# Optimization experiments

Hardware: AMD Instinct MI355X
Metric: run time of the kernel (lower is better)

The kernel has to match this reference:

```python
import jax, jax.numpy as jnp
import numpy as np

B, T, IN, H, NC = 256, 512, 64, 512, 64
H2 = H // 2


def setup_inputs() -> dict:
    key = jax.random.key(0)
    ks = jax.random.split(key, 13)
    s = 0.05
    return {
        "x": jax.random.normal(ks[0], (B, T, IN), jnp.float32),
        # layer 0 LSTM weights (PyTorch layout: [4H, in], gate order i,f,g,o)
        "w_ih0": jax.random.normal(ks[1], (4 * H, IN), jnp.float32) * s,
        "w_hh0": jax.random.normal(ks[2], (4 * H, H), jnp.float32) * s,
        "b_ih0": jax.random.normal(ks[3], (4 * H,), jnp.float32) * s,
        "b_hh0": jax.random.normal(ks[4], (4 * H,), jnp.float32) * s,
        # layer 1 LSTM weights
        "w_ih1": jax.random.normal(ks[5], (4 * H, H), jnp.float32) * s,
        "w_hh1": jax.random.normal(ks[6], (4 * H, H), jnp.float32) * s,
        "b_ih1": jax.random.normal(ks[7], (4 * H,), jnp.float32) * s,
        "b_hh1": jax.random.normal(ks[8], (4 * H,), jnp.float32) * s,
        # classifier head
        "w1": jax.random.normal(ks[9], (H2, H), jnp.float32) * s,
        "b1": jax.random.normal(ks[10], (H2,), jnp.float32) * s,
        "w2": jax.random.normal(ks[11], (NC, H2), jnp.float32) * s,
        "b2": jax.random.normal(ks[12], (NC,), jnp.float32) * s,
    }


def _lstm_layer(x, w_ih, w_hh, b_ih, b_hh):
    # x: [B, T, D_in] -> hidden sequence [B, T, H]
    b, t, _ = x.shape
    h_dim = w_hh.shape[1]
    # precompute input projection for all time steps: [B, T, 4H]
    gx = jnp.einsum('btd,gd->btg', x, w_ih) + b_ih + b_hh

    def step(carry, g_t):
        h, c = carry
        gates = g_t + h @ w_hh.T  # [B, 4H]
        i, f, g, o = jnp.split(gates, 4, axis=-1)
        i = jax.nn.sigmoid(i)
        f = jax.nn.sigmoid(f)
        g = jnp.tanh(g)
        o = jax.nn.sigmoid(o)
        c_new = f * c + i * g
        h_new = o * jnp.tanh(c_new)
        return (h_new, c_new), h_new

    h0 = jnp.zeros((b, h_dim), x.dtype)
    c0 = jnp.zeros((b, h_dim), x.dtype)
    (_, _), hs = jax.lax.scan(step, (h0, c0), jnp.swapaxes(gx, 0, 1))
    return jnp.swapaxes(hs, 0, 1)  # [B, T, H]


def reference(x, w_ih0, w_hh0, b_ih0, b_hh0, w_ih1, w_hh1, b_ih1, b_hh1, w1, b1, w2, b2):
    # 2-layer LSTM (eval mode: inter-layer dropout disabled)
    out = _lstm_layer(x, w_ih0, w_hh0, b_ih0, b_hh0)
    out = _lstm_layer(out, w_ih1, w_hh1, b_ih1, b_hh1)
    feat = out[:, -1, :]  # last time step hidden state [B, H]
    # classifier: Linear -> ReLU -> (Dropout off in eval) -> Linear
    hmid = jax.nn.relu(feat @ w1.T + b1)
    logits = hmid @ w2.T + b2
    return logits
```

## Files before the change

### kernel.cpp

```cpp
#include <hip/hip_runtime.h>
#include <stdint.h>

#define B_  256
#define T_  512
#define IN_ 64
#define H_  512
#define G4_ 2048
#define NC_ 64
#define H2_ 256

typedef _Float16 f16;
typedef __attribute__((ext_vector_type(4))) _Float16 f16x4;
typedef __attribute__((ext_vector_type(4))) float    f32x4;
typedef __attribute__((ext_vector_type(4))) unsigned int u32x4;

__device__ __forceinline__ float sigf(float x) {
  return __builtin_amdgcn_rcpf(1.0f + __expf(-x));
}
__device__ __forceinline__ float tanh_fast(float x) {
  x = fminf(fmaxf(x, -15.f), 15.f);
  const float e = __expf(2.f * x);
  return (e - 1.f) * __builtin_amdgcn_rcpf(e + 1.f);
}

__device__ __forceinline__ void store_u32_l3(void* p, unsigned v) {
  asm volatile("global_store_dword %0, %1, off sc0 sc1" :: "v"(p), "v"(v) : "memory");
}
__device__ __forceinline__ unsigned load_u32_l3(const void* p) {
  unsigned r;
  asm volatile("global_load_dword %0, %1, off sc0 sc1" : "=v"(r) : "v"(p) : "memory");
  return r;
}
__device__ __forceinline__ u32x4 load_u32x4_l3(const void* p) {
  u32x4 r;
  asm volatile("global_load_dwordx4 %0, %1, off sc0 sc1" : "=v"(r) : "v"(p) : "memory");
  return r;
}
__device__ __forceinline__ void wait_vm0() {
  asm volatile("s_waitcnt vmcnt(0)" ::: "memory");
}

__global__ void cvt_f32_f16(const float* __restrict__ s, f16* __restrict__ d, int n) {
  int i = blockIdx.x * blockDim.x + threadIdx.x;
  int st = gridDim.x * blockDim.x;
  for (; i < n; i += st) d[i] = (f16)s[i];
}

__global__ void bias_comb(const float* __restrict__ a, const float* __restrict__ b,
                          float* __restrict__ d, int n) {
  int i = blockIdx.x * blockDim.x + threadIdx.x;
  if (i < n) d[i] = a[i] + b[i];
}

__global__ __launch_bounds__(512, 2) void fused_g(
    const f16* __restrict__ x16,
    const f16* __restrict__ wih0,
    const f16* __restrict__ whh0,
    const f16* __restrict__ wih1,
    const f16* __restrict__ whh1,
    const float* __restrict__ bias0,
    const float* __restrict__ bias1,
    f16* __restrict__ h0seq,
    f16* __restrict__ hbuf1,
    unsigned* __restrict__ flags) {
  __shared__ __align__(16) unsigned char smem[50688];
  const int bid = blockIdx.x;
  const int tid = threadIdx.x;
  const int lane = tid & 63, wv = tid >> 6;
  const int l15 = lane & 15, hi = lane >> 4;

  if (bid < 128) {
    const int grp = bid >> 3, sl = bid & 7;
    f16 (*xt)[72]   = (f16(*)[72])smem;
    f16 (*ht)[532]  = (f16(*)[532])(smem + 2304);
    float (*gl)[260] = (float(*)[260])(smem + 2304 + 17024);

    int gidx[2]; f16x4 bhh[2][32]; f16x4 bih[2][4]; float bv[2];
#pragma unroll
    for (int nt = 0; nt < 2; ++nt) {
      const int lg = (wv * 2 + nt) * 16 + l15;
      const int grow = (lg >> 6) * H_ + sl * 64 + (lg & 63);
      gidx[nt] = grow; bv[nt] = bias0[grow];
      const f16* wp = whh0 + (size_t)grow * H_;
#pragma unroll
      for (int ks = 0; ks < 32; ++ks) bhh[nt][ks] = *(const f16x4*)(wp + ks * 16 + 4 * hi);
      const f16* wq = wih0 + (size_t)grow * IN_;
#pragma unroll
      for (int ks = 0; ks < 4; ++ks) bih[nt][ks] = *(const f16x4*)(wq + ks * 16 + 4 * hi);
    }

    const int bl = tid >> 5;
    const int j0 = (tid & 31) * 2;
    float c0 = 0.f, c1 = 0.f;
    const int hrow = tid >> 5, hcol = (tid & 31) * 16;

    for (int t = 0; t < T_; ++t) {
      if (tid < 128) {
        const f16* xs = x16 + ((size_t)(grp * 16 + (tid >> 3)) * T_ + t) * IN_ + (tid & 7) * 8;
        *(uint4*)&xt[tid >> 3][(tid & 7) * 8] = *(const uint4*)xs;
      }
      if (t != 0) {
        const unsigned* pp = flags + (size_t)(grp * 8 + (lane & 7)) * 16;
        const unsigned want = (unsigned)t;
        for (;;) {
          unsigned v = load_u32_l3(pp); wait_vm0();
          if (__all((int)(v >= want))) break;
          __builtin_amdgcn_s_sleep(1);
        }
        const f16* hs = h0seq + ((size_t)(t - 1) * B_ + grp * 16 + hrow) * H_ + hcol;
        u32x4 r0 = load_u32x4_l3(hs);
        u32x4 r1 = load_u32x4_l3(hs + 8);
        wait_vm0();
        __builtin_amdgcn_sched_barrier(0);
        *(u32x4*)&ht[hrow][hcol]     = r0;
        *(u32x4*)&ht[hrow][hcol + 8] = r1;
      } else {
        u32x4 z = {0u, 0u, 0u, 0u};
        *(u32x4*)&ht[hrow][hcol]     = z;
        *(u32x4*)&ht[hrow][hcol + 8] = z;
      }
      __syncthreads();

      f32x4 acc[2];
#pragma unroll
      for (int nt = 0; nt < 2; ++nt) { acc[nt][0] = bv[nt]; acc[nt][1] = bv[nt]; acc[nt][2] = bv[nt]; acc[nt][3] = bv[nt]; }
#pragma unroll
      for (int ks = 0; ks < 4; ++ks) {
        const f16x4 a = *(const f16x4*)&xt[l15][ks * 16 + 4 * hi];
        acc[0] = __builtin_amdgcn_mfma_f32_16x16x16f16(a, bih[0][ks], acc[0], 0, 0, 0);
        acc[1] = __builtin_amdgcn_mfma_f32_16x16x16f16(a, bih[1][ks], acc[1], 0, 0, 0);
      }
#pragma unroll
      for (int ks = 0; ks < 32; ++ks) {
        const f16x4 a = *(const f16x4*)&ht[l15][ks * 16 + 4 * hi];
        acc[0] = __builtin_amdgcn_mfma_f32_16x16x16f16(a, bhh[0][ks], acc[0], 0, 0, 0);
        acc[1] = __builtin_amdgcn_mfma_f32_16x16x16f16(a, bhh[1][ks], acc[1], 0, 0, 0);
      }
#pragma unroll
      for (int nt = 0; nt < 2; ++nt) {
        const int col = (wv * 2 + nt) * 16 + l15;
#pragma unroll
        for (int r = 0; r < 4; ++r) gl[4 * hi + r][col] = acc[nt][r];
      }
      __syncthreads();

      const float gi = gl[bl][j0],        gi1 = gl[bl][j0 + 1];
      const float gf = gl[bl][64 + j0],   gf1 = gl[bl][64 + j0 + 1];
      const float gg = gl[bl][128 + j0],  gg1 = gl[bl][128 + j0 + 1];
      const float go = gl[bl][192 + j0],  go1 = gl[bl][192 + j0 + 1];
      c0 = sigf(gf) * c0 + sigf(gi) * tanh_fast(gg);
      c1 = sigf(gf1) * c1 + sigf(gi1) * tanh_fast(gg1);
      const f16 h0h = (f16)(sigf(go) * tanh_fast(c0));
      const f16 h1h = (f16)(sigf(go1) * tanh_fast(c1));
      unsigned hp = ((unsigned)__builtin_bit_cast(unsigned short, h1h) << 16)
                  |  (unsigned)__builtin_bit_cast(unsigned short, h0h);
      store_u32_l3(h0seq + ((size_t)t * B_ + grp * 16 + bl) * H_ + sl * 64 + j0, hp);
      wait_vm0();
      __syncthreads();
      if (tid == 0) store_u32_l3(flags + (size_t)(grp * 8 + sl) * 16, (unsigned)(t + 1));
    }

  } else {
    const int grp = (bid - 128) >> 3, sl = (bid - 128) & 7;
    f16 (*ht0)[532]  = (f16(*)[532])smem;
    f16 (*ht1)[532]  = (f16(*)[532])(smem + 17024);
    float (*gl)[260] = (float(*)[260])(smem + 34048);

    int gidx[2]; f16x4 bih[2][32]; f16x4 bhh[2][32]; float bv[2];
#pragma unroll
    for (int nt = 0; nt < 2; ++nt) {
      const int lg = (wv * 2 + nt) * 16 + l15;
      const int grow = (lg >> 6) * H_ + sl * 64 + (lg & 63);
      gidx[nt] = grow; bv[nt] = bias1[grow];
      const f16* wp = wih1 + (size_t)grow * H_;
#pragma unroll
      for (int ks = 0; ks < 32; ++ks) bih[nt][ks] = *(const f16x4*)(wp + ks * 16 + 4 * hi);
      const f16* wq = whh1 + (size_t)grow * H_;
#pragma unroll
      for (int ks = 0; ks < 32; ++ks) bhh[nt][ks] = *(const f16x4*)(wq + ks * 16 + 4 * hi);
    }

    const int bl = tid >> 5;
    const int j0 = (tid & 31) * 2;
    float c0 = 0.f, c1 = 0.f;
    const int hrow = tid >> 5, hcol = (tid & 31) * 16;

    for (int t = 0; t < T_; ++t) {
      {
        const bool isOwn = (lane >= 8 && lane < 16);
        const int slot = isOwn ? (128 + grp * 8 + (lane - 8)) : (grp * 8 + (lane & 7));
        const unsigned want = isOwn ? (unsigned)t : (unsigned)(t + 1);
        const unsigned* pp = flags + (size_t)slot * 16;
        for (;;) {
          unsigned v = load_u32_l3(pp); wait_vm0();
          if (__all((int)(v >= want))) break;
          __builtin_amdgcn_s_sleep(1);
        }
      }
      {
        const f16* hs0 = h0seq + ((size_t)t * B_ + grp * 16 + hrow) * H_ + hcol;
        u32x4 r0 = load_u32x4_l3(hs0);
        u32x4 r1 = load_u32x4_l3(hs0 + 8);
        if (t != 0) {
          const f16* hs1 = hbuf1 + ((size_t)((t - 1) & 1) * B_ + grp * 16 + hrow) * H_ + hcol;
          u32x4 r2 = load_u32x4_l3(hs1);
          u32x4 r3 = load_u32x4_l3(hs1 + 8);
          wait_vm0();
          __builtin_amdgcn_sched_barrier(0);
          *(u32x4*)&ht1[hrow][hcol]     = r2;
          *(u32x4*)&ht1[hrow][hcol + 8] = r3;
        } else {
          wait_vm0();
          __builtin_amdgcn_sched_barrier(0);
          u32x4 z = {0u, 0u, 0u, 0u};
          *(u32x4*)&ht1[hrow][hcol]     = z;
          *(u32x4*)&ht1[hrow][hcol + 8] = z;
        }
        *(u32x4*)&ht0[hrow][hcol]     = r0;
        *(u32x4*)&ht0[hrow][hcol + 8] = r1;
      }
      __syncthreads();

      f32x4 acc[2];
#pragma unroll
      for (int nt = 0; nt < 2; ++nt) { acc[nt][0] = bv[nt]; acc[nt][1] = bv[nt]; acc[nt][2] = bv[nt]; acc[nt][3] = bv[nt]; }
#pragma unroll
      for (int ks = 0; ks < 32; ++ks) {
        const f16x4 a0 = *(const f16x4*)&ht0[l15][ks * 16 + 4 * hi];
        acc[0] = __builtin_amdgcn_mfma_f32_16x16x16f16(a0, bih[0][ks], acc[0], 0, 0, 0);
        acc[1] = __builtin_amdgcn_mfma_f32_16x16x16f16(a0, bih[1][ks], acc[1], 0, 0, 0);
      }
#pragma unroll
      for (int ks = 0; ks < 32; ++ks) {
        const f16x4 a1 = *(const f16x4*)&ht1[l15][ks * 16 + 4 * hi];
        acc[0] = __builtin_amdgcn_mfma_f32_16x16x16f16(a1, bhh[0][ks], acc[0], 0, 0, 0);
        acc[1] = __builtin_amdgcn_mfma_f32_16x16x16f16(a1, bhh[1][ks], acc[1], 0, 0, 0);
      }
#pragma unroll
      for (int nt = 0; nt < 2; ++nt) {
        const int col = (wv * 2 + nt) * 16 + l15;
#pragma unroll
        for (int r = 0; r < 4; ++r) gl[4 * hi + r][col] = acc[nt][r];
      }
      __syncthreads();

      const float gi = gl[bl][j0],        gi1 = gl[bl][j0 + 1];
      const float gf = gl[bl][64 + j0],   gf1 = gl[bl][64 + j0 + 1];
      const float gg = gl[bl][128 + j0],  gg1 = gl[bl][128 + j0 + 1];
      const float go = gl[bl][192 + j0],  go1 = gl[bl][192 + j0 + 1];
      c0 = sigf(gf) * c0 + sigf(gi) * tanh_fast(gg);
      c1 = sigf(gf1) * c1 + sigf(gi1) * tanh_fast(gg1);
      const f16 ha = (f16)(sigf(go) * tanh_fast(c0));
      const f16 hb = (f16)(sigf(go1) * tanh_fast(c1));
      unsigned hp = ((unsigned)__builtin_bit_cast(unsigned short, hb) << 16)
                  |  (unsigned)__builtin_bit_cast(unsigned short, ha);
      store_u32_l3(hbuf1 + ((size_t)(t & 1) * B_ + grp * 16 + bl) * H_ + sl * 64 + j0, hp);
      wait_vm0();
      __syncthreads();
      if (tid == 0) store_u32_l3(flags + (size_t)(128 + grp * 8 + sl) * 16, (unsigned)(t + 1));
    }
  }
}

__global__ void head_g(const f16* __restrict__ h1, const float* __restrict__ w1,
                       const float* __restrict__ b1, const float* __restrict__ w2,
                       const float* __restrict__ b2, float* __restrict__ out) {
  __shared__ float ft[512];
  __shared__ float hm[256];
  const int b = blockIdx.x, tid = threadIdx.x;
  ft[tid * 2]     = (float)h1[(size_t)b * H_ + tid * 2];
  ft[tid * 2 + 1] = (float)h1[(size_t)b * H_ + tid * 2 + 1];
  __syncthreads();
  {
    float d = b1[tid];
    const float* wr = w1 + (size_t)tid * H_;
#pragma unroll 8
    for (int k = 0; k < H_; ++k) d += ft[k] * wr[k];
    hm[tid] = fmaxf(d, 0.f);
  }
  __syncthreads();
  if (tid < NC_) {
    float d = b2[tid];
    const float* wr = w2 + (size_t)tid * H2_;
#pragma unroll 8
    for (int k = 0; k < H2_; ++k) d += hm[k] * wr[k];
    out[(size_t)b * NC_ + tid] = d;
  }
}

extern "C" void kernel_launch(void* const* d_in, const int* in_sizes, int n_in,
                              void* d_out, int out_size, void* d_ws, size_t ws_size,
                              hipStream_t stream) {
  const float* x     = (const float*)d_in[0];
  const float* w_ih0 = (const float*)d_in[1];
  const float* w_hh0 = (const float*)d_in[2];
  const float* b_ih0 = (const float*)d_in[3];
  const float* b_hh0 = (const float*)d_in[4];
  const float* w_ih1 = (const float*)d_in[5];
  const float* w_hh1 = (const float*)d_in[6];
  const float* b_ih1 = (const float*)d_in[7];
  const float* b_hh1 = (const float*)d_in[8];
  const float* w1    = (const float*)d_in[9];
  const float* b1    = (const float*)d_in[10];
  const float* w2    = (const float*)d_in[11];
  const float* b2    = (const float*)d_in[12];
  float* out = (float*)d_out;

  char* p = (char*)d_ws;
  auto alloc = [&](size_t bytes) { char* r = p; p += (bytes + 255) & ~(size_t)255; return r; };
  f16*   h0seq  = (f16*)alloc((size_t)T_ * B_ * H_ * 2);
  f16*   hbuf1  = (f16*)alloc((size_t)2 * B_ * H_ * 2);
  f16*   x16    = (f16*)alloc((size_t)B_ * T_ * IN_ * 2);
  f16*   wih0h  = (f16*)alloc((size_t)G4_ * IN_ * 2);
  f16*   whh0h  = (f16*)alloc((size_t)G4_ * H_ * 2);
  f16*   wih1h  = (f16*)alloc((size_t)G4_ * H_ * 2);
  f16*   whh1h  = (f16*)alloc((size_t)G4_ * H_ * 2);
  float* bias0c = (float*)alloc(G4_ * 4);
  float* bias1c = (float*)alloc(G4_ * 4);
  unsigned* flags = (unsigned*)alloc(256 * 64);

  hipMemsetAsync(flags, 0, 256 * 64, stream);
  cvt_f32_f16<<<2048, 256, 0, stream>>>(x, x16, B_ * T_ * IN_);
  cvt_f32_f16<<<512, 256, 0, stream>>>(w_ih0, wih0h, G4_ * IN_);
  cvt_f32_f16<<<2048, 256, 0, stream>>>(w_hh0, whh0h, G4_ * H_);
  cvt_f32_f16<<<2048, 256, 0, stream>>>(w_ih1, wih1h, G4_ * H_);
  cvt_f32_f16<<<2048, 256, 0, stream>>>(w_hh1, whh1h, G4_ * H_);
  bias_comb<<<8, 256, 0, stream>>>(b_ih0, b_hh0, bias0c, G4_);
  bias_comb<<<8, 256, 0, stream>>>(b_ih1, b_hh1, bias1c, G4_);

  fused_g<<<256, 512, 0, stream>>>(x16, wih0h, whh0h, wih1h, whh1h,
                                   bias0c, bias1c, h0seq, hbuf1, flags);
  head_g<<<B_, 256, 0, stream>>>(hbuf1 + (size_t)B_ * H_, w1, b1, w2, b2, out);
}
```

Before: 3.518 ms.

## Split layer-1 wait so input projection overlaps the recurrent dependency

Layer-1 blocks now wait only for the layer-0 flags, then compute the W_ih·h0 MFMAs before waiting on the peer layer-1 flags and loading h1(t-1). This takes the input-projection half off the critical recurrent path. To make room, the W_ih1 fragments are no longer kept in registers but are reloaded from global memory on every step, and the launch bounds change to one block per EU with waves_per_eu set to 2. The exchange is extra global weight traffic per step and one more barrier, in return for a shorter serial dependency chain.

```diff
diff --git a/kernel.cpp b/kernel.cpp
--- a/kernel.cpp
+++ b/kernel.cpp
@@ -52,7 +52,8 @@
   if (i < n) d[i] = a[i] + b[i];
 }
 
-__global__ __launch_bounds__(512, 2) void fused_g(
+__global__ __launch_bounds__(512, 1) __attribute__((amdgpu_waves_per_eu(2, 2)))
+void fused_g(
     const f16* __restrict__ x16,
     const f16* __restrict__ wih0,
     const f16* __restrict__ whh0,
@@ -166,15 +167,14 @@
     f16 (*ht1)[532]  = (f16(*)[532])(smem + 17024);
     float (*gl)[260] = (float(*)[260])(smem + 34048);
 
-    int gidx[2]; f16x4 bih[2][32]; f16x4 bhh[2][32]; float bv[2];
+    int gidx[2]; f16x4 bhh[2][32]; float bv[2];
+    const f16* wih_p[2];
 #pragma unroll
     for (int nt = 0; nt < 2; ++nt) {
       const int lg = (wv * 2 + nt) * 16 + l15;
       const int grow = (lg >> 6) * H_ + sl * 64 + (lg & 63);
       gidx[nt] = grow; bv[nt] = bias1[grow];
-      const f16* wp = wih1 + (size_t)grow * H_;
-#pragma unroll
-      for (int ks = 0; ks < 32; ++ks) bih[nt][ks] = *(const f16x4*)(wp + ks * 16 + 4 * hi);
+      wih_p[nt] = wih1 + (size_t)grow * H_ + 4 * hi;
       const f16* wq = whh1 + (size_t)grow * H_;
 #pragma unroll
       for (int ks = 0; ks < 32; ++ks) bhh[nt][ks] = *(const f16x4*)(wq + ks * 16 + 4 * hi);
@@ -187,35 +187,18 @@
 
     for (int t = 0; t < T_; ++t) {
       {
-        const bool isOwn = (lane >= 8 && lane < 16);
-        const int slot = isOwn ? (128 + grp * 8 + (lane - 8)) : (grp * 8 + (lane & 7));
-        const unsigned want = isOwn ? (unsigned)t : (unsigned)(t + 1);
-        const unsigned* pp = flags + (size_t)slot * 16;
+        const unsigned* pp = flags + (size_t)(grp * 8 + (lane & 7)) * 16;
+        const unsigned want = (unsigned)(t + 1);
         for (;;) {
           unsigned v = load_u32_l3(pp); wait_vm0();
           if (__all((int)(v >= want))) break;
           __builtin_amdgcn_s_sleep(1);
         }
-      }
-      {
         const f16* hs0 = h0seq + ((size_t)t * B_ + grp * 16 + hrow) * H_ + hcol;
         u32x4 r0 = load_u32x4_l3(hs0);
         u32x4 r1 = load_u32x4_l3(hs0 + 8);
-        if (t != 0) {
-          const f16* hs1 = hbuf1 + ((size_t)((t - 1) & 1) * B_ + grp * 16 + hrow) * H_ + hcol;
-          u32x4 r2 = load_u32x4_l3(hs1);
-          u32x4 r3 = load_u32x4_l3(hs1 + 8);
-          wait_vm0();
-          __builtin_amdgcn_sched_barrier(0);
-          *(u32x4*)&ht1[hrow][hcol]     = r2;
-          *(u32x4*)&ht1[hrow][hcol + 8] = r3;
-        } else {
-          wait_vm0();
-          __builtin_amdgcn_sched_barrier(0);
-          u32x4 z = {0u, 0u, 0u, 0u};
-          *(u32x4*)&ht1[hrow][hcol]     = z;
-          *(u32x4*)&ht1[hrow][hcol + 8] = z;
-        }
+        wait_vm0();
+        __builtin_amdgcn_sched_barrier(0);
         *(u32x4*)&ht0[hrow][hcol]     = r0;
         *(u32x4*)&ht0[hrow][hcol + 8] = r1;
       }
@@ -227,9 +210,34 @@
 #pragma unroll
       for (int ks = 0; ks < 32; ++ks) {
         const f16x4 a0 = *(const f16x4*)&ht0[l15][ks * 16 + 4 * hi];
-        acc[0] = __builtin_amdgcn_mfma_f32_16x16x16f16(a0, bih[0][ks], acc[0], 0, 0, 0);
-        acc[1] = __builtin_amdgcn_mfma_f32_16x16x16f16(a0, bih[1][ks], acc[1], 0, 0, 0);
-      }
+        const f16x4 w0 = *(const f16x4*)(wih_p[0] + ks * 16);
+        const f16x4 w1 = *(const f16x4*)(wih_p[1] + ks * 16);
+        acc[0] = __builtin_amdgcn_mfma_f32_16x16x16f16(a0, w0, acc[0], 0, 0, 0);
+        acc[1] = __builtin_amdgcn_mfma_f32_16x16x16f16(a0, w1, acc[1], 0, 0, 0);
+      }
+
+      if (t != 0) {
+        const unsigned* pp = flags + (size_t)(128 + grp * 8 + (lane & 7)) * 16;
+        const unsigned want = (unsigned)t;
+        for (;;) {
+          unsigned v = load_u32_l3(pp); wait_vm0();
+          if (__all((int)(v >= want))) break;
+          __builtin_amdgcn_s_sleep(1);
+        }
+        const f16* hs1 = hbuf1 + ((size_t)((t - 1) & 1) * B_ + grp * 16 + hrow) * H_ + hcol;
+        u32x4 r2 = load_u32x4_l3(hs1);
+        u32x4 r3 = load_u32x4_l3(hs1 + 8);
+        wait_vm0();
+        __builtin_amdgcn_sched_barrier(0);
+        *(u32x4*)&ht1[hrow][hcol]     = r2;
+        *(u32x4*)&ht1[hrow][hcol + 8] = r3;
+      } else {
+        u32x4 z = {0u, 0u, 0u, 0u};
+        *(u32x4*)&ht1[hrow][hcol]     = z;
+        *(u32x4*)&ht1[hrow][hcol + 8] = z;
+      }
+      __syncthreads();
+
 #pragma unroll
       for (int ks = 0; ks < 32; ++ks) {
         const f16x4 a1 = *(const f16x4*)&ht1[l15][ks * 16 + 4 * hi];
```

Result: slower. 9.051 ms (+157.3%).

## Repartition LSTM blocks to 32 batch rows by 32 hidden units, stream weights

Applied to the files above, without the earlier changes.

Each block now handles 32 batch rows and a 32-unit hidden slice (128 gate rows) instead of 16 rows by 64 units. Groups grow from 8 to 16 blocks, so each flag poll covers 16 flags. Weights are no longer held in registers; each MFMA k-step loads its weight fragment from global memory and reuses it for two batch M-tiles. This frees registers and halves the weight columns per block, but adds per-step global weight loads, a larger LDS footprint that may limit occupancy, and twice as many producers for each group to wait on.

```diff
diff --git a/kernel.cpp b/kernel.cpp
--- a/kernel.cpp
+++ b/kernel.cpp
@@ -63,201 +63,207 @@
     f16* __restrict__ h0seq,
     f16* __restrict__ hbuf1,
     unsigned* __restrict__ flags) {
-  __shared__ __align__(16) unsigned char smem[50688];
+  __shared__ __align__(16) unsigned char smem[85504];
   const int bid = blockIdx.x;
   const int tid = threadIdx.x;
   const int lane = tid & 63, wv = tid >> 6;
   const int l15 = lane & 15, hi = lane >> 4;
 
+  const int rb = (bid < 128) ? bid : (bid - 128);
+  const int k8 = rb >> 3;
+  const int sl = ((rb & 7) << 1) | (k8 & 1);
+  const int grp = k8 >> 1;
+
+  const int lg = wv * 16 + l15;
+  const int grow = (lg >> 5) * H_ + sl * 32 + (lg & 31);
+  const int row = tid >> 4;
+  const int j0 = (tid & 15) * 2;
+  const int hrow = tid >> 4, hcol = (tid & 15) * 32;
+
   if (bid < 128) {
-    const int grp = bid >> 3, sl = bid & 7;
-    f16 (*xt)[72]   = (f16(*)[72])smem;
-    f16 (*ht)[532]  = (f16(*)[532])(smem + 2304);
-    float (*gl)[260] = (float(*)[260])(smem + 2304 + 17024);
-
-    int gidx[2]; f16x4 bhh[2][32]; f16x4 bih[2][4]; float bv[2];
-#pragma unroll
-    for (int nt = 0; nt < 2; ++nt) {
-      const int lg = (wv * 2 + nt) * 16 + l15;
-      const int grow = (lg >> 6) * H_ + sl * 64 + (lg & 63);
-      gidx[nt] = grow; bv[nt] = bias0[grow];
-      const f16* wp = whh0 + (size_t)grow * H_;
-#pragma unroll
-      for (int ks = 0; ks < 32; ++ks) bhh[nt][ks] = *(const f16x4*)(wp + ks * 16 + 4 * hi);
-      const f16* wq = wih0 + (size_t)grow * IN_;
-#pragma unroll
-      for (int ks = 0; ks < 4; ++ks) bih[nt][ks] = *(const f16x4*)(wq + ks * 16 + 4 * hi);
-    }
-
-    const int bl = tid >> 5;
-    const int j0 = (tid & 31) * 2;
+    f16 (*xt)[72]    = (f16(*)[72])smem;
+    f16 (*ht)[536]   = (f16(*)[536])(smem + 4608);
+    float (*gl)[132] = (float(*)[132])(smem + 4608 + 34304);
+
+    const float bv = bias0[grow];
+    const f16* wihp = wih0 + (size_t)grow * IN_ + 4 * hi;
+    const f16* whhp = whh0 + (size_t)grow * H_ + 4 * hi;
+
     float c0 = 0.f, c1 = 0.f;
-    const int hrow = tid >> 5, hcol = (tid & 31) * 16;
 
     for (int t = 0; t < T_; ++t) {
-      if (tid < 128) {
-        const f16* xs = x16 + ((size_t)(grp * 16 + (tid >> 3)) * T_ + t) * IN_ + (tid & 7) * 8;
+      if (tid < 256) {
+        const f16* xs = x16 + ((size_t)(grp * 32 + (tid >> 3)) * T_ + t) * IN_ + (tid & 7) * 8;
         *(uint4*)&xt[tid >> 3][(tid & 7) * 8] = *(const uint4*)xs;
       }
       if (t != 0) {
-        const unsigned* pp = flags + (size_t)(grp * 8 + (lane & 7)) * 16;
+        const unsigned* pp = flags + (size_t)(grp * 16 + (lane & 15)) * 16;
         const unsigned want = (unsigned)t;
         for (;;) {
           unsigned v = load_u32_l3(pp); wait_vm0();
           if (__all((int)(v >= want))) break;
           __builtin_amdgcn_s_sleep(1);
         }
-        const f16* hs = h0seq + ((size_t)(t - 1) * B_ + grp * 16 + hrow) * H_ + hcol;
+        const f16* hs = h0seq + ((size_t)(t - 1) * B_ + grp * 32 + hrow) * H_ + hcol;
         u32x4 r0 = load_u32x4_l3(hs);
         u32x4 r1 = load_u32x4_l3(hs + 8);
+        u32x4 r2 = load_u32x4_l3(hs + 16);
+        u32x4 r3 = load_u32x4_l3(hs + 24);
         wait_vm0();
         __builtin_amdgcn_sched_barrier(0);
-        *(u32x4*)&ht[hrow][hcol]     = r0;
-        *(u32x4*)&ht[hrow][hcol + 8] = r1;
+        *(u32x4*)&ht[hrow][hcol]      = r0;
+        *(u32x4*)&ht[hrow][hcol + 8]  = r1;
+        *(u32x4*)&ht[hrow][hcol + 16] = r2;
+        *(u32x4*)&ht[hrow][hcol + 24] = r3;
       } else {
         u32x4 z = {0u, 0u, 0u, 0u};
-        *(u32x4*)&ht[hrow][hcol]     = z;
-        *(u32x4*)&ht[hrow][hcol + 8] = z;
+        *(u32x4*)&ht[hrow][hcol]      = z;
+        *(u32x4*)&ht[hrow][hcol + 8]  = z;
+        *(u32x4*)&ht[hrow][hcol + 16] = z;
+        *(u32x4*)&ht[hrow][hcol + 24] = z;
       }
       __syncthreads();
 
       f32x4 acc[2];
-#pragma unroll
-      for (int nt = 0; nt < 2; ++nt) { acc[nt][0] = bv[nt]; acc[nt][1] = bv[nt]; acc[nt][2] = bv[nt]; acc[nt][3] = bv[nt]; }
+      acc[0][0] = bv; acc[0][1] = bv; acc[0][2] = bv; acc[0][3] = bv;
+      acc[1] = acc[0];
 #pragma unroll
       for (int ks = 0; ks < 4; ++ks) {
-        const f16x4 a = *(const f16x4*)&xt[l15][ks * 16 + 4 * hi];
-        acc[0] = __builtin_amdgcn_mfma_f32_16x16x16f16(a, bih[0][ks], acc[0], 0, 0, 0);
-        acc[1] = __builtin_amdgcn_mfma_f32_16x16x16f16(a, bih[1][ks], acc[1], 0, 0, 0);
+        const f16x4 a0 = *(const f16x4*)&xt[l15][ks * 16 + 4 * hi];
+        const f16x4 a1 = *(const f16x4*)&xt[16 + l15][ks * 16 + 4 * hi];
+        const f16x4 w  = *(const f16x4*)(wihp + ks * 16);
+        acc[0] = __builtin_amdgcn_mfma_f32_16x16x16f16(a0, w, acc[0], 0, 0, 0);
+        acc[1] = __builtin_amdgcn_mfma_f32_16x16x16f16(a1, w, acc[1], 0, 0, 0);
       }
 #pragma unroll
       for (int ks = 0; ks < 32; ++ks) {
-        const f16x4 a = *(const f16x4*)&ht[l15][ks * 16 + 4 * hi];
-        acc[0] = __builtin_amdgcn_mfma_f32_16x16x16f16(a, bhh[0][ks], acc[0], 0, 0, 0);
-        acc[1] = __builtin_amdgcn_mfma_f32_16x16x16f16(a, bhh[1][ks], acc[1], 0, 0, 0);
-      }
-#pragma unroll
-      for (int nt = 0; nt < 2; ++nt) {
-        const int col = (wv * 2 + nt) * 16 + l15;
-#pragma unroll
-        for (int r = 0; r < 4; ++r) gl[4 * hi + r][col] = acc[nt][r];
-      }
-      __syncthreads();
-
-      const float gi = gl[bl][j0],        gi1 = gl[bl][j0 + 1];
-      const float gf = gl[bl][64 + j0],   gf1 = gl[bl][64 + j0 + 1];
-      const float gg = gl[bl][128 + j0],  gg1 = gl[bl][128 + j0 + 1];
-      const float go = gl[bl][192 + j0],  go1 = gl[bl][192 + j0 + 1];
-      c0 = sigf(gf) * c0 + sigf(gi) * tanh_fast(gg);
-      c1 = sigf(gf1) * c1 + sigf(gi1) * tanh_fast(gg1);
-      const f16 h0h = (f16)(sigf(go) * tanh_fast(c0));
-      const f16 h1h = (f16)(sigf(go1) * tanh_fast(c1));
-      unsigned hp = ((unsigned)__builtin_bit_cast(unsigned short, h1h) << 16)
-                  |  (unsigned)__builtin_bit_cast(unsigned short, h0h);
-      store_u32_l3(h0seq + ((size_t)t * B_ + grp * 16 + bl) * H_ + sl * 64 + j0, hp);
-      wait_vm0();
-      __syncthreads();
-      if (tid == 0) store_u32_l3(flags + (size_t)(grp * 8 + sl) * 16, (unsigned)(t + 1));
-    }
-
-  } else {
-    const int grp = (bid - 128) >> 3, sl = (bid - 128) & 7;
-    f16 (*ht0)[532]  = (f16(*)[532])smem;
-    f16 (*ht1)[532]  = (f16(*)[532])(smem + 17024);
-    float (*gl)[260] = (float(*)[260])(smem + 34048);
-
-    int gidx[2]; f16x4 bih[2][32]; f16x4 bhh[2][32]; float bv[2];
-#pragma unroll
-    for (int nt = 0; nt < 2; ++nt) {
-      const int lg = (wv * 2 + nt) * 16 + l15;
-      const int grow = (lg >> 6) * H_ + sl * 64 + (lg & 63);
-      gidx[nt] = grow; bv[nt] = bias1[grow];
-      const f16* wp = wih1 + (size_t)grow * H_;
-#pragma unroll
-      for (int ks = 0; ks < 32; ++ks) bih[nt][ks] = *(const f16x4*)(wp + ks * 16 + 4 * hi);
-      const f16* wq = whh1 + (size_t)grow * H_;
-#pragma unroll
-      for (int ks = 0; ks < 32; ++ks) bhh[nt][ks] = *(const f16x4*)(wq + ks * 16 + 4 * hi);
-    }
-
-    const int bl = tid >> 5;
-    const int j0 = (tid & 31) * 2;
-    float c0 = 0.f, c1 = 0.f;
-    const int hrow = tid >> 5, hcol = (tid & 31) * 16;
-
-    for (int t = 0; t < T_; ++t) {
-      {
-        const bool isOwn = (lane >= 8 && lane < 16);
-        const int slot = isOwn ? (128 + grp * 8 + (lane - 8)) : (grp * 8 + (lane & 7));
-        const unsigned want = isOwn ? (unsigned)t : (unsigned)(t + 1);
-        const unsigned* pp = flags + (size_t)slot * 16;
-        for (;;) {
-          unsigned v = load_u32_l3(pp); wait_vm0();
-          if (__all((int)(v >= want))) break;
-          __builtin_amdgcn_s_sleep(1);
-        }
-      }
-      {
-        const f16* hs0 = h0seq + ((size_t)t * B_ + grp * 16 + hrow) * H_ + hcol;
-        u32x4 r0 = load_u32x4_l3(hs0);
-        u32x4 r1 = load_u32x4_l3(hs0 + 8);
-        if (t != 0) {
-          const f16* hs1 = hbuf1 + ((size_t)((t - 1) & 1) * B_ + grp * 16 + hrow) * H_ + hcol;
-          u32x4 r2 = load_u32x4_l3(hs1);
-          u32x4 r3 = load_u32x4_l3(hs1 + 8);
-          wait_vm0();
-          __builtin_amdgcn_sched_barrier(0);
-          *(u32x4*)&ht1[hrow][hcol]     = r2;
-          *(u32x4*)&ht1[hrow][hcol + 8] = r3;
-        } else {
-          wait_vm0();
-          __builtin_amdgcn_sched_barrier(0);
-          u32x4 z = {0u, 0u, 0u, 0u};
-          *(u32x4*)&ht1[hrow][hcol]     = z;
-          *(u32x4*)&ht1[hrow][hcol + 8] = z;
-        }
-        *(u32x4*)&ht0[hrow][hcol]     = r0;
-        *(u32x4*)&ht0[hrow][hcol + 8] = r1;
-      }
-      __syncthreads();
-
-      f32x4 acc[2];
-#pragma unroll
-      for (int nt = 0; nt < 2; ++nt) { acc[nt][0] = bv[nt]; acc[nt][1] = bv[nt]; acc[nt][2] = bv[nt]; acc[nt][3] = bv[nt]; }
-#pragma unroll
-      for (int ks = 0; ks < 32; ++ks) {
-        const f16x4 a0 = *(const f16x4*)&ht0[l15][ks * 16 + 4 * hi];
-        acc[0] = __builtin_amdgcn_mfma_f32_16x16x16f16(a0, bih[0][ks], acc[0], 0, 0, 0);
-        acc[1] = __builtin_amdgcn_mfma_f32_16x16x16f16(a0, bih[1][ks], acc[1], 0, 0, 0);
-      }
-#pragma unroll
-      for (int ks = 0; ks < 32; ++ks) {
-        const f16x4 a1 = *(const f16x4*)&ht1[l15][ks * 16 + 4 * hi];
-        acc[0] = __builtin_amdgcn_mfma_f32_16x16x16f16(a1, bhh[0][ks], acc[0], 0, 0, 0);
-        acc[1] = __builtin_amdgcn_mfma_f32_16x16x16f16(a1, bhh[1][ks], acc[1], 0, 0, 0);
-      }
-#pragma unroll
-      for (int nt = 0; nt < 2; ++nt) {
-        const int col = (wv * 2 + nt) * 16 + l15;
-#pragma unroll
-        for (int r = 0; r < 4; ++r) gl[4 * hi + r][col] = acc[nt][r];
-      }
-      __syncthreads();
-
-      const float gi = gl[bl][j0],        gi1 = gl[bl][j0 + 1];
-      const float gf = gl[bl][64 + j0],   gf1 = gl[bl][64 + j0 + 1];
-      const float gg = gl[bl][128 + j0],  gg1 = gl[bl][128 + j0 + 1];
-      const float go = gl[bl][192 + j0],  go1 = gl[bl][192 + j0 + 1];
+        const f16x4 a0 = *(const f16x4*)&ht[l15][ks * 16 + 4 * hi];
+        const f16x4 a1 = *(const f16x4*)&ht[16 + l15][ks * 16 + 4 * hi];
+        const f16x4 w  = *(const f16x4*)(whhp + ks * 16);
+        acc[0] = __builtin_amdgcn_mfma_f32_16x16x16f16(a0, w, acc[0], 0, 0, 0);
+        acc[1] = __builtin_amdgcn_mfma_f32_16x16x16f16(a1, w, acc[1], 0, 0, 0);
+      }
+      const int col = wv * 16 + l15;
+#pragma unroll
+      for (int mt = 0; mt < 2; ++mt)
+#pragma unroll
+        for (int r = 0; r < 4; ++r) gl[mt * 16 + 4 * hi + r][col] = acc[mt][r];
+      __syncthreads();
+
+      const float gi = gl[row][j0],       gi1 = gl[row][j0 + 1];
+      const float gf = gl[row][32 + j0],  gf1 = gl[row][32 + j0 + 1];
+      const float gg = gl[row][64 + j0],  gg1 = gl[row][64 + j0 + 1];
+      const float go = gl[row][96 + j0],  go1 = gl[row][96 + j0 + 1];
       c0 = sigf(gf) * c0 + sigf(gi) * tanh_fast(gg);
       c1 = sigf(gf1) * c1 + sigf(gi1) * tanh_fast(gg1);
       const f16 ha = (f16)(sigf(go) * tanh_fast(c0));
       const f16 hb = (f16)(sigf(go1) * tanh_fast(c1));
       unsigned hp = ((unsigned)__builtin_bit_cast(unsigned short, hb) << 16)
                   |  (unsigned)__builtin_bit_cast(unsigned short, ha);
-      store_u32_l3(hbuf1 + ((size_t)(t & 1) * B_ + grp * 16 + bl) * H_ + sl * 64 + j0, hp);
+      store_u32_l3(h0seq + ((size_t)t * B_ + grp * 32 + row) * H_ + sl * 32 + j0, hp);
       wait_vm0();
       __syncthreads();
-      if (tid == 0) store_u32_l3(flags + (size_t)(128 + grp * 8 + sl) * 16, (unsigned)(t + 1));
+      if (tid == 0) store_u32_l3(flags + (size_t)(grp * 16 + sl) * 16, (unsigned)(t + 1));
+    }
+
+  } else {
+    f16 (*ht0)[536]  = (f16(*)[536])smem;
+    f16 (*ht1)[536]  = (f16(*)[536])(smem + 34304);
+    float (*gl)[132] = (float(*)[132])(smem + 68608);
+
+    const float bv = bias1[grow];
+    const f16* wihp = wih1 + (size_t)grow * H_ + 4 * hi;
+    const f16* whhp = whh1 + (size_t)grow * H_ + 4 * hi;
+
+    float c0 = 0.f, c1 = 0.f;
+
+    for (int t = 0; t < T_; ++t) {
+      {
+        const int la = lane & 31;
+        const unsigned* pp;
+        unsigned want;
+        if (la < 16) { pp = flags + (size_t)(grp * 16 + la) * 16;        want = (unsigned)(t + 1); }
+        else         { pp = flags + (size_t)(128 + grp * 16 + (la - 16)) * 16; want = (unsigned)t; }
+        for (;;) {
+          unsigned v = load_u32_l3(pp); wait_vm0();
+          if (__all((int)(v >= want))) break;
+          __builtin_amdgcn_s_sleep(1);
+        }
+      }
+      {
+        const f16* hs0 = h0seq + ((size_t)t * B_ + grp * 32 + hrow) * H_ + hcol;
+        u32x4 r0 = load_u32x4_l3(hs0);
+        u32x4 r1 = load_u32x4_l3(hs0 + 8);
+        u32x4 r2 = load_u32x4_l3(hs0 + 16);
+        u32x4 r3 = load_u32x4_l3(hs0 + 24);
+        if (t != 0) {
+          const f16* hs1 = hbuf1 + ((size_t)((t - 1) & 1) * B_ + grp * 32 + hrow) * H_ + hcol;
+          u32x4 s0 = load_u32x4_l3(hs1);
+          u32x4 s1 = load_u32x4_l3(hs1 + 8);
+          u32x4 s2 = load_u32x4_l3(hs1 + 16);
+          u32x4 s3 = load_u32x4_l3(hs1 + 24);
+          wait_vm0();
+          __builtin_amdgcn_sched_barrier(0);
+          *(u32x4*)&ht1[hrow][hcol]      = s0;
+          *(u32x4*)&ht1[hrow][hcol + 8]  = s1;
+          *(u32x4*)&ht1[hrow][hcol + 16] = s2;
+          *(u32x4*)&ht1[hrow][hcol + 24] = s3;
+        } else {
+          wait_vm0();
+          __builtin_amdgcn_sched_barrier(0);
+          u32x4 z = {0u, 0u, 0u, 0u};
+          *(u32x4*)&ht1[hrow][hcol]      = z;
+          *(u32x4*)&ht1[hrow][hcol + 8]  = z;
+          *(u32x4*)&ht1[hrow][hcol + 16] = z;
+          *(u32x4*)&ht1[hrow][hcol + 24] = z;
+        }
+        *(u32x4*)&ht0[hrow][hcol]      = r0;
+        *(u32x4*)&ht0[hrow][hcol + 8]  = r1;
+        *(u32x4*)&ht0[hrow][hcol + 16] = r2;
+        *(u32x4*)&ht0[hrow][hcol + 24] = r3;
+      }
+      __syncthreads();
+
+      f32x4 acc[2];
+      acc[0][0] = bv; acc[0][1] = bv; acc[0][2] = bv; acc[0][3] = bv;
+      acc[1] = acc[0];
+#pragma unroll
+      for (int ks = 0; ks < 32; ++ks) {
+        const f16x4 a0 = *(const f16x4*)&ht0[l15][ks * 16 + 4 * hi];
+        const f16x4 a1 = *(const f16x4*)&ht0[16 + l15][ks * 16 + 4 * hi];
+        const f16x4 w  = *(const f16x4*)(wihp + ks * 16);
+        acc[0] = __builtin_amdgcn_mfma_f32_16x16x16f16(a0, w, acc[0], 0, 0, 0);
+        acc[1] = __builtin_amdgcn_mfma_f32_16x16x16f16(a1, w, acc[1], 0, 0, 0);
+      }
+#pragma unroll
+      for (int ks = 0; ks < 32; ++ks) {
+        const f16x4 a0 = *(const f16x4*)&ht1[l15][ks * 16 + 4 * hi];
+        const f16x4 a1 = *(const f16x4*)&ht1[16 + l15][ks * 16 + 4 * hi];
+        const f16x4 w  = *(const f16x4*)(whhp + ks * 16);
+        acc[0] = __builtin_amdgcn_mfma_f32_16x16x16f16(a0, w, acc[0], 0, 0, 0);
+        acc[1] = __builtin_amdgcn_mfma_f32_16x16x16f16(a1, w, acc[1], 0, 0, 0);
+      }
+      const int col = wv * 16 + l15;
+#pragma unroll
+      for (int mt = 0; mt < 2; ++mt)
+#pragma unroll
+        for (int r = 0; r < 4; ++r) gl[mt * 16 + 4 * hi + r][col] = acc[mt][r];
+      __syncthreads();
+
+      const float gi = gl[row][j0],       gi1 = gl[row][j0 + 1];
+      const float gf = gl[row][32 + j0],  gf1 = gl[row][32 + j0 + 1];
+      const float gg = gl[row][64 + j0],  gg1 = gl[row][64 + j0 + 1];
+      const float go = gl[row][96 + j0],  go1 = gl[row][96 + j0 + 1];
+      c0 = sigf(gf) * c0 + sigf(gi) * tanh_fast(gg);
+      c1 = sigf(gf1) * c1 + sigf(gi1) * tanh_fast(gg1);
+      const f16 ha = (f16)(sigf(go) * tanh_fast(c0));
+      const f16 hb = (f16)(sigf(go1) * tanh_fast(c1));
+      unsigned hp = ((unsigned)__builtin_bit_cast(unsigned short, hb) << 16)
+                  |  (unsigned)__builtin_bit_cast(unsigned short, ha);
+      store_u32_l3(hbuf1 + ((size_t)(t & 1) * B_ + grp * 32 + row) * H_ + sl * 32 + j0, hp);
+      wait_vm0();
+      __syncthreads();
+      if (tid == 0) store_u32_l3(flags + (size_t)(128 + grp * 16 + sl) * 16, (unsigned)(t + 1));
     }
   }
 }
```

After: 9.376 ms. 2.66x slower.
